# Kernel optimization log

Measured on AMD Instinct MI355X. Metric: run time of the kernel, lower is better.

The kernel has to match this reference:

```python
import jax, jax.numpy as jnp
import numpy as np

N_NODES = 50000
N_EDGES = 600000
IN_DIM, HID, OUT_DIM = 128, 128, 64
LN_EPS = 1e-5


def setup_inputs() -> dict:
    key = jax.random.key(0)
    ks = jax.random.split(key, 10)
    def glorot(k, shape):
        lim = np.sqrt(6.0 / (shape[0] + shape[1]))
        return jax.random.uniform(k, shape, jnp.float32, -lim, lim)
    return {
        "x": jax.random.normal(ks[0], (N_NODES, IN_DIM), jnp.float32),
        "src": jax.random.randint(ks[1], (N_EDGES,), 0, N_NODES, jnp.int32),
        "dst": jax.random.randint(ks[2], (N_EDGES,), 0, N_NODES, jnp.int32),
        "W0": glorot(ks[3], (IN_DIM, HID)), "b0": jnp.zeros((HID,), jnp.float32),
        "W1": glorot(ks[4], (HID, HID)),    "b1": jnp.zeros((HID,), jnp.float32),
        "W2": glorot(ks[5], (HID, OUT_DIM)),"b2": jnp.zeros((OUT_DIM,), jnp.float32),
        "ln_scale": jnp.ones((HID,), jnp.float32),
        "ln_bias": jnp.zeros((HID,), jnp.float32),
    }


def _degree_norms(src, dst):
    ones = jnp.ones((src.shape[0],), jnp.float32)
    deg_out = jax.ops.segment_sum(ones, src, num_segments=N_NODES)
    deg_in = jax.ops.segment_sum(ones, dst, num_segments=N_NODES)
    # DGL clamps degree to min 1 for norm='both'
    out_norm = jnp.clip(deg_out, 1.0, None) ** -0.5
    in_norm = jnp.clip(deg_in, 1.0, None) ** -0.5
    return out_norm, in_norm


def _graph_conv(h, src, dst, out_norm, in_norm, W, b):
    # norm='both': scale src side, SpMM aggregate, scale dst side, then affine
    h = h * out_norm[:, None]
    h = h @ W  # apply weight first (mathematically identical, smaller messages when out<in)
    agg = jax.ops.segment_sum(h[src], dst, num_segments=N_NODES)  # [N, D]
    return agg * in_norm[:, None] + b


def _layernorm(h, scale, bias):
    mu = jnp.mean(h, axis=-1, keepdims=True)
    var = jnp.var(h, axis=-1, keepdims=True)
    return (h - mu) * jax.lax.rsqrt(var + LN_EPS) * scale + bias


def reference(x, src, dst, W0, b0, W1, b1, W2, b2, ln_scale, ln_bias):
    out_norm, in_norm = _degree_norms(src, dst)
    # dropout is identity in eval mode
    h = jax.nn.relu(_graph_conv(x, src, dst, out_norm, in_norm, W0, b0))
    h = _layernorm(h, ln_scale, ln_bias)
    h = jax.nn.relu(_graph_conv(h, src, dst, out_norm, in_norm, W1, b1))
    h = _layernorm(h, ln_scale, ln_bias)
    # last layer: encoding=True -> keep activation; no norm after last layer
    h = jax.nn.relu(_graph_conv(h, src, dst, out_norm, in_norm, W2, b2))
    return h
```

## Files before the change

kernel.cpp:

```cpp
#include <hip/hip_runtime.h>
#include <hip/hip_fp16.h>

#define NN 50000
#define NE 600000
#define LN_EPS 1e-5f
#define SCAN_B 49
#define RANGES 8
#define RSZ 6250
#define CHUNKS 30
#define CSZ 20000

typedef __attribute__((ext_vector_type(8))) _Float16 half8;
typedef __attribute__((ext_vector_type(4))) float floatx4;

__device__ __align__(16) __half g_h0[NN * 128];
__device__ __align__(16) __half g_h1[NN * 128];
__device__ float g_out_norm[NN];
__device__ float g_in_norm[NN];
__device__ int g_rowptr[NN + 1];
__device__ int g_esrc[NE];
__device__ int g_blocksum[SCAN_B];
__device__ int g_pout[CHUNKS * NN];
__device__ int g_pin[CHUNKS * NN];
__device__ int g_base[CHUNKS * NN];
__device__ unsigned g_bar_count = 0;
__device__ unsigned g_bar_gen = 0;

__device__ __forceinline__ __half* hbuf(int i) { return i ? g_h1 : g_h0; }

__device__ __forceinline__ void gridbar(unsigned* expected) {
    __syncthreads();
    if (threadIdx.x == 0) {
        __threadfence();
        unsigned prev = __hip_atomic_fetch_add(&g_bar_count, 1u, __ATOMIC_ACQ_REL,
                                               __HIP_MEMORY_SCOPE_AGENT);
        if (prev == gridDim.x - 1) {
            __hip_atomic_store(&g_bar_count, 0u, __ATOMIC_RELAXED, __HIP_MEMORY_SCOPE_AGENT);
            __hip_atomic_fetch_add(&g_bar_gen, 1u, __ATOMIC_RELEASE, __HIP_MEMORY_SCOPE_AGENT);
        } else {
            while (__hip_atomic_load(&g_bar_gen, __ATOMIC_ACQUIRE, __HIP_MEMORY_SCOPE_AGENT) ==
                   *expected)
                __builtin_amdgcn_s_sleep(8);
        }
        __threadfence();
    }
    __syncthreads();
    (*expected)++;
}

__global__ __launch_bounds__(256) void histo_kernel(const int* __restrict__ src,
                                                    const int* __restrict__ dst) {
    __shared__ int h_out[RSZ];
    __shared__ int h_in[RSZ];
    int c = blockIdx.x / RANGES, r = blockIdx.x % RANGES;
    int lo = r * RSZ;
    for (int i = threadIdx.x; i < RSZ; i += 256) { h_out[i] = 0; h_in[i] = 0; }
    __syncthreads();
    const int4* s4 = (const int4*)(src + c * CSZ);
    const int4* d4 = (const int4*)(dst + c * CSZ);
    for (int i = threadIdx.x; i < CSZ / 4; i += 256) {
        int4 s = s4[i], d = d4[i];
        int v;
        v = s.x - lo; if ((unsigned)v < RSZ) atomicAdd(&h_out[v], 1);
        v = s.y - lo; if ((unsigned)v < RSZ) atomicAdd(&h_out[v], 1);
        v = s.z - lo; if ((unsigned)v < RSZ) atomicAdd(&h_out[v], 1);
        v = s.w - lo; if ((unsigned)v < RSZ) atomicAdd(&h_out[v], 1);
        v = d.x - lo; if ((unsigned)v < RSZ) atomicAdd(&h_in[v], 1);
        v = d.y - lo; if ((unsigned)v < RSZ) atomicAdd(&h_in[v], 1);
        v = d.z - lo; if ((unsigned)v < RSZ) atomicAdd(&h_in[v], 1);
        v = d.w - lo; if ((unsigned)v < RSZ) atomicAdd(&h_in[v], 1);
    }
    __syncthreads();
    for (int i = threadIdx.x; i < RSZ; i += 256) {
        g_pout[c * NN + lo + i] = h_out[i];
        g_pin[c * NN + lo + i]  = h_in[i];
    }
}

__global__ __launch_bounds__(1024) void mid_kernel() {
    __shared__ int sums[1024];
    __shared__ int aux[64];
    unsigned expected = __hip_atomic_load(&g_bar_gen, __ATOMIC_RELAXED, __HIP_MEMORY_SCOPE_AGENT);
    int b = blockIdx.x, t = threadIdx.x;
    int n = b * 1024 + t;
    int si = 0;
    if (n < NN) {
        int so = 0;
#pragma unroll
        for (int c = 0; c < CHUNKS; ++c) { so += g_pout[c * NN + n]; si += g_pin[c * NN + n]; }
        g_out_norm[n] = rsqrtf((float)max(so, 1));
        g_in_norm[n]  = rsqrtf((float)max(si, 1));
    }
    int s = si;
#pragma unroll
    for (int off = 32; off; off >>= 1) s += __shfl_xor(s, off, 64);
    if ((t & 63) == 0) aux[t >> 6] = s;
    __syncthreads();
    if (t < 16) {
        int v = aux[t];
#pragma unroll
        for (int off = 8; off; off >>= 1) v += __shfl_xor(v, off, 16);
        if (t == 0) g_blocksum[b] = v;
    }
    gridbar(&expected);
    if (t < 64) {
        int own = (t < SCAN_B) ? g_blocksum[t] : 0;
        int v = own;
#pragma unroll
        for (int off = 1; off < 64; off <<= 1) {
            int nb = __shfl_up(v, off, 64);
            if (t >= off) v += nb;
        }
        aux[t] = v - own;
        if (b == 0 && t == SCAN_B - 1) g_rowptr[NN] = v;
    }
    __syncthreads();
    int blockoff = aux[b];
    sums[t] = si;
    __syncthreads();
    for (int off = 1; off < 1024; off <<= 1) {
        int add = (t >= off) ? sums[t - off] : 0;
        __syncthreads();
        sums[t] += add;
        __syncthreads();
    }
    int excl = sums[t] - si + blockoff;
    if (n < NN) {
        g_rowptr[n] = excl;
        int run = excl;
#pragma unroll
        for (int c = 0; c < CHUNKS; ++c) {
            g_base[c * NN + n] = run;
            run += g_pin[c * NN + n];
        }
    }
}

__global__ __launch_bounds__(256) void place_lds_kernel(const int* __restrict__ src,
                                                        const int* __restrict__ dst) {
    __shared__ int cur[RSZ];
    int c = blockIdx.x / RANGES, r = blockIdx.x % RANGES;
    int lo = r * RSZ;
    for (int i = threadIdx.x; i < RSZ; i += 256) cur[i] = g_base[c * NN + lo + i];
    __syncthreads();
    const int4* s4 = (const int4*)(src + c * CSZ);
    const int4* d4 = (const int4*)(dst + c * CSZ);
    for (int i = threadIdx.x; i < CSZ / 4; i += 256) {
        int4 s = s4[i], d = d4[i];
        int v, p;
        v = d.x - lo; if ((unsigned)v < RSZ) { p = atomicAdd(&cur[v], 1); g_esrc[p] = s.x; }
        v = d.y - lo; if ((unsigned)v < RSZ) { p = atomicAdd(&cur[v], 1); g_esrc[p] = s.y; }
        v = d.z - lo; if ((unsigned)v < RSZ) { p = atomicAdd(&cur[v], 1); g_esrc[p] = s.z; }
        v = d.w - lo; if ((unsigned)v < RSZ) { p = atomicAdd(&cur[v], 1); g_esrc[p] = s.w; }
    }
}

template <int N, bool AEXT>
__global__ __launch_bounds__(256) void gemm_mfma(const float* __restrict__ Aext,
                                                 int a_ib, int c_ib,
                                                 const float* __restrict__ Wg,
                                                 int M) {
    constexpr int NT = N / 16;
    constexpr int LOGN = (N == 128) ? 7 : 6;
    __shared__ _Float16 Wl[128 * N];

    const int tid = threadIdx.x;
    for (int e = tid; e < 128 * N; e += 256) {
        int k = e >> LOGN, n = e & (N - 1);
        Wl[(((k >> 3) * N + n) << 3) + (k & 7)] = (_Float16)Wg[e];
    }
    __syncthreads();

    const int wv = tid >> 6, lane = tid & 63;
    const int quad = lane >> 4, mrow = lane & 15;
    const int rowbase = blockIdx.x * 64 + wv * 16;
    const int arow0 = rowbase + mrow;
    const int arow = (arow0 < M) ? arow0 : (M - 1);

    floatx4 acc[NT] = {};
    const __half* Ah = AEXT ? nullptr : hbuf(a_ib);

#pragma unroll
    for (int kk = 0; kk < 4; ++kk) {
        const int k0 = kk * 32 + quad * 8;
        half8 afrag;
        if (AEXT) {
            const float4* ap = (const float4*)(Aext + (size_t)arow * 128 + k0);
            float4 f0 = ap[0], f1 = ap[1];
            afrag[0] = (_Float16)f0.x; afrag[1] = (_Float16)f0.y;
            afrag[2] = (_Float16)f0.z; afrag[3] = (_Float16)f0.w;
            afrag[4] = (_Float16)f1.x; afrag[5] = (_Float16)f1.y;
            afrag[6] = (_Float16)f1.z; afrag[7] = (_Float16)f1.w;
        } else {
            afrag = *(const half8*)(Ah + (size_t)arow * 128 + k0);
        }
#pragma unroll
        for (int nt = 0; nt < NT; ++nt) {
            half8 bfrag = *(const half8*)&Wl[(((kk * 4 + quad) * N + nt * 16 + mrow) << 3)];
            acc[nt] = __builtin_amdgcn_mfma_f32_16x16x32_f16(afrag, bfrag, acc[nt], 0, 0, 0);
        }
    }

    __half* C = hbuf(c_ib);
#pragma unroll
    for (int r = 0; r < 4; ++r) {
        int crow = rowbase + quad * 4 + r;
        if (crow < M) {
            float s = g_out_norm[crow];
#pragma unroll
            for (int nt = 0; nt < NT; ++nt) {
                float v = acc[nt][r] * s;
                C[(size_t)crow * N + nt * 16 + mrow] = __float2half_rn(v);
            }
        }
    }
}

__global__ __launch_bounds__(256) void gather_ln_kernel(int s_ib, int d_ib,
                                                        const float* __restrict__ b,
                                                        const float* __restrict__ ln_s,
                                                        const float* __restrict__ ln_b) {
    int wave = threadIdx.x >> 6;
    int lane = threadIdx.x & 63;
    int sub = lane >> 5, sl = lane & 31;
    int node = blockIdx.x * 8 + wave * 2 + sub;
    const uint2* Hu = (const uint2*)hbuf(s_ib);
    int beg = g_rowptr[node], end = g_rowptr[node + 1];
    float a0 = 0.f, a1 = 0.f, a2 = 0.f, a3 = 0.f;
    int j = beg;
    for (; j + 3 < end; j += 4) {
        int s0 = g_esrc[j], s1 = g_esrc[j + 1], s2 = g_esrc[j + 2], s3 = g_esrc[j + 3];
        uint2 u0 = Hu[s0 * 32 + sl];
        uint2 u1 = Hu[s1 * 32 + sl];
        uint2 u2 = Hu[s2 * 32 + sl];
        uint2 u3 = Hu[s3 * 32 + sl];
        float2 p0 = __half22float2(*(const __half2*)&u0.x), q0 = __half22float2(*(const __half2*)&u0.y);
        float2 p1 = __half22float2(*(const __half2*)&u1.x), q1 = __half22float2(*(const __half2*)&u1.y);
        float2 p2 = __half22float2(*(const __half2*)&u2.x), q2 = __half22float2(*(const __half2*)&u2.y);
        float2 p3 = __half22float2(*(const __half2*)&u3.x), q3 = __half22float2(*(const __half2*)&u3.y);
        a0 += (p0.x + p1.x) + (p2.x + p3.x);
        a1 += (p0.y + p1.y) + (p2.y + p3.y);
        a2 += (q0.x + q1.x) + (q2.x + q3.x);
        a3 += (q0.y + q1.y) + (q2.y + q3.y);
    }
    for (; j < end; ++j) {
        uint2 u = Hu[g_esrc[j] * 32 + sl];
        float2 p = __half22float2(*(const __half2*)&u.x), q = __half22float2(*(const __half2*)&u.y);
        a0 += p.x; a1 += p.y; a2 += q.x; a3 += q.y;
    }
    float nrm = g_in_norm[node];
    float4 bb = ((const float4*)b)[sl];
    float v0 = fmaxf(a0 * nrm + bb.x, 0.f);
    float v1 = fmaxf(a1 * nrm + bb.y, 0.f);
    float v2 = fmaxf(a2 * nrm + bb.z, 0.f);
    float v3 = fmaxf(a3 * nrm + bb.w, 0.f);
    float s = (v0 + v1) + (v2 + v3);
    float sq = (v0 * v0 + v1 * v1) + (v2 * v2 + v3 * v3);
#pragma unroll
    for (int off = 16; off > 0; off >>= 1) {
        s  += __shfl_xor(s, off, 64);
        sq += __shfl_xor(sq, off, 64);
    }
    float mean = s * (1.f / 128.f);
    float var = sq * (1.f / 128.f) - mean * mean;
    float inv = rsqrtf(var + LN_EPS);
    float4 ls = ((const float4*)ln_s)[sl];
    float4 lb = ((const float4*)ln_b)[sl];
    float o0 = (v0 - mean) * inv * ls.x + lb.x;
    float o1 = (v1 - mean) * inv * ls.y + lb.y;
    float o2 = (v2 - mean) * inv * ls.z + lb.z;
    float o3 = (v3 - mean) * inv * ls.w + lb.w;
    __half2 h0 = __floats2half2_rn(o0, o1);
    __half2 h1 = __floats2half2_rn(o2, o3);
    uint2 o = make_uint2(*(const unsigned int*)&h0, *(const unsigned int*)&h1);
    ((uint2*)hbuf(d_ib))[node * 32 + sl] = o;
}

__global__ __launch_bounds__(256) void GCN_63831803953156_kernel(int s_ib,
                                                                 const float* __restrict__ b2,
                                                                 float* __restrict__ out) {
    int wave = threadIdx.x >> 6;
    int lane = threadIdx.x & 63;
    int sub = lane >> 4, sl = lane & 15;
    int node = blockIdx.x * 16 + wave * 4 + sub;
    const uint2* Hu = (const uint2*)hbuf(s_ib);
    int beg = g_rowptr[node], end = g_rowptr[node + 1];
    float a0 = 0.f, a1 = 0.f, a2 = 0.f, a3 = 0.f;
    int j = beg;
    for (; j + 3 < end; j += 4) {
        int s0 = g_esrc[j], s1 = g_esrc[j + 1], s2 = g_esrc[j + 2], s3 = g_esrc[j + 3];
        uint2 u0 = Hu[s0 * 16 + sl];
        uint2 u1 = Hu[s1 * 16 + sl];
        uint2 u2 = Hu[s2 * 16 + sl];
        uint2 u3 = Hu[s3 * 16 + sl];
        float2 p0 = __half22float2(*(const __half2*)&u0.x), q0 = __half22float2(*(const __half2*)&u0.y);
        float2 p1 = __half22float2(*(const __half2*)&u1.x), q1 = __half22float2(*(const __half2*)&u1.y);
        float2 p2 = __half22float2(*(const __half2*)&u2.x), q2 = __half22float2(*(const __half2*)&u2.y);
        float2 p3 = __half22float2(*(const __half2*)&u3.x), q3 = __half22float2(*(const __half2*)&u3.y);
        a0 += (p0.x + p1.x) + (p2.x + p3.x);
        a1 += (p0.y + p1.y) + (p2.y + p3.y);
        a2 += (q0.x + q1.x) + (q2.x + q3.x);
        a3 += (q0.y + q1.y) + (q2.y + q3.y);
    }
    for (; j < end; ++j) {
        uint2 u = Hu[g_esrc[j] * 16 + sl];
        float2 p = __half22float2(*(const __half2*)&u.x), q = __half22float2(*(const __half2*)&u.y);
        a0 += p.x; a1 += p.y; a2 += q.x; a3 += q.y;
    }
    float nrm = g_in_norm[node];
    float4 bb = ((const float4*)b2)[sl];
    float4 o;
    o.x = fmaxf(a0 * nrm + bb.x, 0.f);
    o.y = fmaxf(a1 * nrm + bb.y, 0.f);
    o.z = fmaxf(a2 * nrm + bb.z, 0.f);
    o.w = fmaxf(a3 * nrm + bb.w, 0.f);
    ((float4*)out)[node * 16 + sl] = o;
}

extern "C" void kernel_launch(void* const* d_in, const int* in_sizes, int n_in,
                              void* d_out, int out_size, void* d_ws, size_t ws_size,
                              hipStream_t stream) {
    const float* x   = (const float*)d_in[0];
    const int* src   = (const int*)d_in[1];
    const int* dst   = (const int*)d_in[2];
    const float* W0  = (const float*)d_in[3];
    const float* b0  = (const float*)d_in[4];
    const float* W1  = (const float*)d_in[5];
    const float* b1  = (const float*)d_in[6];
    const float* W2  = (const float*)d_in[7];
    const float* b2  = (const float*)d_in[8];
    const float* ln_s = (const float*)d_in[9];
    const float* ln_b = (const float*)d_in[10];
    (void)d_ws; (void)ws_size; (void)in_sizes; (void)n_in; (void)out_size;

    histo_kernel<<<CHUNKS * RANGES, 256, 0, stream>>>(src, dst);
    mid_kernel<<<SCAN_B, 1024, 0, stream>>>();
    place_lds_kernel<<<CHUNKS * RANGES, 256, 0, stream>>>(src, dst);

    const int GB = (NN + 63) / 64;

    gemm_mfma<128, true><<<GB, 256, 0, stream>>>(x, -1, 0, W0, NN);
    gather_ln_kernel<<<NN / 8, 256, 0, stream>>>(0, 1, b0, ln_s, ln_b);

    gemm_mfma<128, false><<<GB, 256, 0, stream>>>(nullptr, 1, 0, W1, NN);
    gather_ln_kernel<<<NN / 8, 256, 0, stream>>>(0, 1, b1, ln_s, ln_b);

    gemm_mfma<64, false><<<GB, 256, 0, stream>>>(nullptr, 1, 0, W2, NN);
    GCN_63831803953156_kernel<<<NN / 16, 256, 0, stream>>>(0, b2, (float*)d_out);
}
```

Before: 252.6 us.

## Degree-sort nodes for gather kernels and widen per-lane loads to 16 bytes

Adds a per-block histogram and counting sort of nodes by in-degree inside mid_kernel, producing a permutation that the gather kernels use so that neighbouring node groups in a wave have similar degrees. This reduces divergence and tail imbalance in the edge loops. The gather kernels also switch from 8-byte to 16-byte loads per lane, which halves the lanes per node and doubles the nodes per wave. In exchange, mid_kernel takes on extra histogram, scan and atomic work, and output writes become scattered by permutation order.

```diff
diff --git a/kernel.cpp b/kernel.cpp
--- a/kernel.cpp
+++ b/kernel.cpp
@@ -20,6 +20,8 @@
 __device__ int g_rowptr[NN + 1];
 __device__ int g_esrc[NE];
 __device__ int g_blocksum[SCAN_B];
+__device__ int g_perm[NN];
+__device__ int g_dhist[SCAN_B * 256];
 __device__ int g_pout[CHUNKS * NN];
 __device__ int g_pin[CHUNKS * NN];
 __device__ int g_base[CHUNKS * NN];
@@ -80,9 +82,12 @@
 __global__ __launch_bounds__(1024) void mid_kernel() {
     __shared__ int sums[1024];
     __shared__ int aux[64];
+    __shared__ int hist[256];
+    __shared__ int cursor[256];
     unsigned expected = __hip_atomic_load(&g_bar_gen, __ATOMIC_RELAXED, __HIP_MEMORY_SCOPE_AGENT);
     int b = blockIdx.x, t = threadIdx.x;
     int n = b * 1024 + t;
+    if (t < 256) hist[t] = 0;
     int si = 0;
     if (n < NN) {
         int so = 0;
@@ -91,11 +96,15 @@
         g_out_norm[n] = rsqrtf((float)max(so, 1));
         g_in_norm[n]  = rsqrtf((float)max(si, 1));
     }
+    __syncthreads();
+    int bin = min(si, 255);
+    if (n < NN) atomicAdd(&hist[bin], 1);
     int s = si;
 #pragma unroll
     for (int off = 32; off; off >>= 1) s += __shfl_xor(s, off, 64);
     if ((t & 63) == 0) aux[t >> 6] = s;
     __syncthreads();
+    if (t < 256) g_dhist[b * 256 + t] = hist[t];
     if (t < 16) {
         int v = aux[t];
 #pragma unroll
@@ -133,6 +142,28 @@
             g_base[c * NN + n] = run;
             run += g_pin[c * NN + n];
         }
+    }
+    int cur = 0, tot = 0;
+    if (t < 256) {
+        for (int b2 = 0; b2 < SCAN_B; ++b2) {
+            int h = g_dhist[b2 * 256 + t];
+            if (b2 < b) cur += h;
+            tot += h;
+        }
+        cursor[t] = tot;
+    }
+    __syncthreads();
+    for (int off = 1; off < 256; off <<= 1) {
+        int add = (t < 256 && t >= off) ? cursor[t - off] : 0;
+        __syncthreads();
+        if (t < 256) cursor[t] += add;
+        __syncthreads();
+    }
+    if (t < 256) cursor[t] = cursor[t] - tot + cur;
+    __syncthreads();
+    if (n < NN) {
+        int pos = atomicAdd(&cursor[bin], 1);
+        g_perm[pos] = n;
     }
 }
 
@@ -216,64 +247,65 @@
     }
 }
 
+#define ACC8(u) { \
+    float2 f0 = __half22float2(*(const __half2*)&(u).x); \
+    float2 f1 = __half22float2(*(const __half2*)&(u).y); \
+    float2 f2 = __half22float2(*(const __half2*)&(u).z); \
+    float2 f3 = __half22float2(*(const __half2*)&(u).w); \
+    a0 += f0.x; a1 += f0.y; a2 += f1.x; a3 += f1.y; \
+    a4 += f2.x; a5 += f2.y; a6 += f3.x; a7 += f3.y; }
+
 __global__ __launch_bounds__(256) void gather_ln_kernel(int s_ib, int d_ib,
                                                         const float* __restrict__ b,
                                                         const float* __restrict__ ln_s,
                                                         const float* __restrict__ ln_b) {
     int wave = threadIdx.x >> 6;
     int lane = threadIdx.x & 63;
-    int sub = lane >> 5, sl = lane & 31;
-    int node = blockIdx.x * 8 + wave * 2 + sub;
-    const uint2* Hu = (const uint2*)hbuf(s_ib);
+    int sub = lane >> 4, sl = lane & 15;
+    int idx = blockIdx.x * 16 + wave * 4 + sub;
+    int node = g_perm[idx];
+    const uint4* Hu = (const uint4*)hbuf(s_ib);
     int beg = g_rowptr[node], end = g_rowptr[node + 1];
-    float a0 = 0.f, a1 = 0.f, a2 = 0.f, a3 = 0.f;
+    float a0 = 0.f, a1 = 0.f, a2 = 0.f, a3 = 0.f, a4 = 0.f, a5 = 0.f, a6 = 0.f, a7 = 0.f;
     int j = beg;
     for (; j + 3 < end; j += 4) {
         int s0 = g_esrc[j], s1 = g_esrc[j + 1], s2 = g_esrc[j + 2], s3 = g_esrc[j + 3];
-        uint2 u0 = Hu[s0 * 32 + sl];
-        uint2 u1 = Hu[s1 * 32 + sl];
-        uint2 u2 = Hu[s2 * 32 + sl];
-        uint2 u3 = Hu[s3 * 32 + sl];
-        float2 p0 = __half22float2(*(const __half2*)&u0.x), q0 = __half22float2(*(const __half2*)&u0.y);
-        float2 p1 = __half22float2(*(const __half2*)&u1.x), q1 = __half22float2(*(const __half2*)&u1.y);
-        float2 p2 = __half22float2(*(const __half2*)&u2.x), q2 = __half22float2(*(const __half2*)&u2.y);
-        float2 p3 = __half22float2(*(const __half2*)&u3.x), q3 = __half22float2(*(const __half2*)&u3.y);
-        a0 += (p0.x + p1.x) + (p2.x + p3.x);
-        a1 += (p0.y + p1.y) + (p2.y + p3.y);
-        a2 += (q0.x + q1.x) + (q2.x + q3.x);
-        a3 += (q0.y + q1.y) + (q2.y + q3.y);
+        uint4 u0 = Hu[s0 * 16 + sl];
+        uint4 u1 = Hu[s1 * 16 + sl];
+        uint4 u2 = Hu[s2 * 16 + sl];
+        uint4 u3 = Hu[s3 * 16 + sl];
+        ACC8(u0); ACC8(u1); ACC8(u2); ACC8(u3);
     }
     for (; j < end; ++j) {
-        uint2 u = Hu[g_esrc[j] * 32 + sl];
-        float2 p = __half22float2(*(const __half2*)&u.x), q = __half22float2(*(const __half2*)&u.y);
-        a0 += p.x; a1 += p.y; a2 += q.x; a3 += q.y;
+        uint4 u = Hu[g_esrc[j] * 16 + sl];
+        ACC8(u);
     }
     float nrm = g_in_norm[node];
-    float4 bb = ((const float4*)b)[sl];
-    float v0 = fmaxf(a0 * nrm + bb.x, 0.f);
-    float v1 = fmaxf(a1 * nrm + bb.y, 0.f);
-    float v2 = fmaxf(a2 * nrm + bb.z, 0.f);
-    float v3 = fmaxf(a3 * nrm + bb.w, 0.f);
-    float s = (v0 + v1) + (v2 + v3);
-    float sq = (v0 * v0 + v1 * v1) + (v2 * v2 + v3 * v3);
-#pragma unroll
-    for (int off = 16; off > 0; off >>= 1) {
+    float4 bA = ((const float4*)b)[sl * 2], bB = ((const float4*)b)[sl * 2 + 1];
+    float v0 = fmaxf(a0 * nrm + bA.x, 0.f), v1 = fmaxf(a1 * nrm + bA.y, 0.f);
+    float v2 = fmaxf(a2 * nrm + bA.z, 0.f), v3 = fmaxf(a3 * nrm + bA.w, 0.f);
+    float v4 = fmaxf(a4 * nrm + bB.x, 0.f), v5 = fmaxf(a5 * nrm + bB.y, 0.f);
+    float v6 = fmaxf(a6 * nrm + bB.z, 0.f), v7 = fmaxf(a7 * nrm + bB.w, 0.f);
+    float s = ((v0 + v1) + (v2 + v3)) + ((v4 + v5) + (v6 + v7));
+    float sq = ((v0 * v0 + v1 * v1) + (v2 * v2 + v3 * v3)) +
+               ((v4 * v4 + v5 * v5) + (v6 * v6 + v7 * v7));
+#pragma unroll
+    for (int off = 8; off > 0; off >>= 1) {
         s  += __shfl_xor(s, off, 64);
         sq += __shfl_xor(sq, off, 64);
     }
     float mean = s * (1.f / 128.f);
     float var = sq * (1.f / 128.f) - mean * mean;
     float inv = rsqrtf(var + LN_EPS);
-    float4 ls = ((const float4*)ln_s)[sl];
-    float4 lb = ((const float4*)ln_b)[sl];
-    float o0 = (v0 - mean) * inv * ls.x + lb.x;
-    float o1 = (v1 - mean) * inv * ls.y + lb.y;
-    float o2 = (v2 - mean) * inv * ls.z + lb.z;
-    float o3 = (v3 - mean) * inv * ls.w + lb.w;
-    __half2 h0 = __floats2half2_rn(o0, o1);
-    __half2 h1 = __floats2half2_rn(o2, o3);
-    uint2 o = make_uint2(*(const unsigned int*)&h0, *(const unsigned int*)&h1);
-    ((uint2*)hbuf(d_ib))[node * 32 + sl] = o;
+    float4 lsA = ((const float4*)ln_s)[sl * 2], lsB = ((const float4*)ln_s)[sl * 2 + 1];
+    float4 lbA = ((const float4*)ln_b)[sl * 2], lbB = ((const float4*)ln_b)[sl * 2 + 1];
+    __half2 h0 = __floats2half2_rn((v0 - mean) * inv * lsA.x + lbA.x, (v1 - mean) * inv * lsA.y + lbA.y);
+    __half2 h1 = __floats2half2_rn((v2 - mean) * inv * lsA.z + lbA.z, (v3 - mean) * inv * lsA.w + lbA.w);
+    __half2 h2 = __floats2half2_rn((v4 - mean) * inv * lsB.x + lbB.x, (v5 - mean) * inv * lsB.y + lbB.y);
+    __half2 h3 = __floats2half2_rn((v6 - mean) * inv * lsB.z + lbB.z, (v7 - mean) * inv * lsB.w + lbB.w);
+    uint4 o = make_uint4(*(const unsigned int*)&h0, *(const unsigned int*)&h1,
+                         *(const unsigned int*)&h2, *(const unsigned int*)&h3);
+    ((uint4*)hbuf(d_ib))[node * 16 + sl] = o;
 }
 
 __global__ __launch_bounds__(256) void GCN_63831803953156_kernel(int s_ib,
@@ -281,40 +313,35 @@
                                                                  float* __restrict__ out) {
     int wave = threadIdx.x >> 6;
     int lane = threadIdx.x & 63;
-    int sub = lane >> 4, sl = lane & 15;
-    int node = blockIdx.x * 16 + wave * 4 + sub;
-    const uint2* Hu = (const uint2*)hbuf(s_ib);
+    int sub = lane >> 3, sl = lane & 7;
+    int idx = blockIdx.x * 32 + wave * 8 + sub;
+    if (idx >= NN) return;
+    int node = g_perm[idx];
+    const uint4* Hu = (const uint4*)hbuf(s_ib);
     int beg = g_rowptr[node], end = g_rowptr[node + 1];
-    float a0 = 0.f, a1 = 0.f, a2 = 0.f, a3 = 0.f;
+    float a0 = 0.f, a1 = 0.f, a2 = 0.f, a3 = 0.f, a4 = 0.f, a5 = 0.f, a6 = 0.f, a7 = 0.f;
     int j = beg;
     for (; j + 3 < end; j += 4) {
         int s0 = g_esrc[j], s1 = g_esrc[j + 1], s2 = g_esrc[j + 2], s3 = g_esrc[j + 3];
-        uint2 u0 = Hu[s0 * 16 + sl];
-        uint2 u1 = Hu[s1 * 16 + sl];
-        uint2 u2 = Hu[s2 * 16 + sl];
-        uint2 u3 = Hu[s3 * 16 + sl];
-        float2 p0 = __half22float2(*(const __half2*)&u0.x), q0 = __half22float2(*(const __half2*)&u0.y);
-        float2 p1 = __half22float2(*(const __half2*)&u1.x), q1 = __half22float2(*(const __half2*)&u1.y);
-        float2 p2 = __half22float2(*(const __half2*)&u2.x), q2 = __half22float2(*(const __half2*)&u2.y);
-        float2 p3 = __half22float2(*(const __half2*)&u3.x), q3 = __half22float2(*(const __half2*)&u3.y);
-        a0 += (p0.x + p1.x) + (p2.x + p3.x);
-        a1 += (p0.y + p1.y) + (p2.y + p3.y);
-        a2 += (q0.x + q1.x) + (q2.x + q3.x);
-        a3 += (q0.y + q1.y) + (q2.y + q3.y);
+        uint4 u0 = Hu[s0 * 8 + sl];
+        uint4 u1 = Hu[s1 * 8 + sl];
+        uint4 u2 = Hu[s2 * 8 + sl];
+        uint4 u3 = Hu[s3 * 8 + sl];
+        ACC8(u0); ACC8(u1); ACC8(u2); ACC8(u3);
     }
     for (; j < end; ++j) {
-        uint2 u = Hu[g_esrc[j] * 16 + sl];
-        float2 p = __half22float2(*(const __half2*)&u.x), q = __half22float2(*(const __half2*)&u.y);
-        a0 += p.x; a1 += p.y; a2 += q.x; a3 += q.y;
+        uint4 u = Hu[g_esrc[j] * 8 + sl];
+        ACC8(u);
     }
     float nrm = g_in_norm[node];
-    float4 bb = ((const float4*)b2)[sl];
-    float4 o;
-    o.x = fmaxf(a0 * nrm + bb.x, 0.f);
-    o.y = fmaxf(a1 * nrm + bb.y, 0.f);
-    o.z = fmaxf(a2 * nrm + bb.z, 0.f);
-    o.w = fmaxf(a3 * nrm + bb.w, 0.f);
-    ((float4*)out)[node * 16 + sl] = o;
+    float4 bA = ((const float4*)b2)[sl * 2], bB = ((const float4*)b2)[sl * 2 + 1];
+    float4 oA, oB;
+    oA.x = fmaxf(a0 * nrm + bA.x, 0.f); oA.y = fmaxf(a1 * nrm + bA.y, 0.f);
+    oA.z = fmaxf(a2 * nrm + bA.z, 0.f); oA.w = fmaxf(a3 * nrm + bA.w, 0.f);
+    oB.x = fmaxf(a4 * nrm + bB.x, 0.f); oB.y = fmaxf(a5 * nrm + bB.y, 0.f);
+    oB.z = fmaxf(a6 * nrm + bB.z, 0.f); oB.w = fmaxf(a7 * nrm + bB.w, 0.f);
+    ((float4*)out)[node * 16 + sl * 2] = oA;
+    ((float4*)out)[node * 16 + sl * 2 + 1] = oB;
 }
 
 extern "C" void kernel_launch(void* const* d_in, const int* in_sizes, int n_in,
@@ -340,11 +367,11 @@
     const int GB = (NN + 63) / 64;
 
     gemm_mfma<128, true><<<GB, 256, 0, stream>>>(x, -1, 0, W0, NN);
-    gather_ln_kernel<<<NN / 8, 256, 0, stream>>>(0, 1, b0, ln_s, ln_b);
+    gather_ln_kernel<<<NN / 16, 256, 0, stream>>>(0, 1, b0, ln_s, ln_b);
 
     gemm_mfma<128, false><<<GB, 256, 0, stream>>>(nullptr, 1, 0, W1, NN);
-    gather_ln_kernel<<<NN / 8, 256, 0, stream>>>(0, 1, b1, ln_s, ln_b);
+    gather_ln_kernel<<<NN / 16, 256, 0, stream>>>(0, 1, b1, ln_s, ln_b);
 
     gemm_mfma<64, false><<<GB, 256, 0, stream>>>(nullptr, 1, 0, W2, NN);
-    GCN_63831803953156_kernel<<<NN / 16, 256, 0, stream>>>(0, b2, (float*)d_out);
-}
+    GCN_63831803953156_kernel<<<(NN + 31) / 32, 256, 0, stream>>>(0, b2, (float*)d_out);
+}
```

New measurement: 244.7 us. 1.03x faster.
